# Kernel tuning notes

Hardware: AMD Instinct MI355X
Metric: run time of the kernel (lower is better)

Reference implementation:

```python
import jax, jax.numpy as jnp
import numpy as np

# Hyperparameters from __init__ defaults / chosen init kwargs
GAMMA_NEG = 4.0
GAMMA_POS = 1.0
CLIP = 0.05
EPS = 1e-8
ALPHA1 = 2.0
ALPHA_OTHER = 0.5
TOP_K = 10

B, C = 2048, 9605


def setup_inputs() -> dict:
    key = jax.random.key(0)
    k_x, k_y, k_c, k_r, k_d, k_o = jax.random.split(key, 6)
    x = jax.random.normal(k_x, (B, C), dtype=jnp.float32)
    y = (jax.random.uniform(k_y, (B, C)) < 0.01).astype(jnp.float32)
    compost_idx = jax.random.randint(k_c, (30,), 0, C, dtype=jnp.int32)
    recycle_idx = jax.random.randint(k_r, (70,), 0, C, dtype=jnp.int32)
    donate_idx = jax.random.randint(k_d, (70,), 0, C, dtype=jnp.int32)
    other_idx = jax.random.randint(k_o, (40,), 0, C, dtype=jnp.int32)
    # dense whitelist mapping: 0 = not in W_human mapping; priority compost>recycle>donate
    wl_map = jnp.zeros((C,), dtype=jnp.int32)
    wl_map = wl_map.at[other_idx].set(4)
    wl_map = wl_map.at[donate_idx].set(3)
    wl_map = wl_map.at[recycle_idx].set(2)
    wl_map = wl_map.at[compost_idx].set(1)
    return {"x": x, "y": y, "compost_idx": compost_idx,
            "recycle_idx": recycle_idx, "donate_idx": donate_idx,
            "wl_map": wl_map}


def reference(x, y, compost_idx, recycle_idx, donate_idx, wl_map):
    b, c = x.shape
    xs_pos = jax.nn.sigmoid(x)
    xs_neg = jnp.minimum(1.0 - xs_pos + CLIP, 1.0)  # clip shift, clamp max=1
    # base asymmetric BCE term: y*log(p) + (1-y)*log(1-p+clip)
    base = (y * jnp.log(jnp.maximum(xs_pos, EPS))
            + (1.0 - y) * jnp.log(jnp.maximum(xs_neg, EPS)))  # [B, C]

    # per-sample ground-truth whitelist groups (find_gt_whitelist)
    has1 = jnp.sum(y[:, compost_idx], axis=1) > 0  # [B]
    has2 = jnp.sum(y[:, recycle_idx], axis=1) > 0
    has3 = jnp.sum(y[:, donate_idx], axis=1) > 0
    gt_only4 = ~(has1 | has2 | has3)  # gt_whitelist == [4]

    # top-10 predicted classes (argsort descending, first 10)
    _, top_idx = jax.lax.top_k(xs_pos, TOP_K)  # [B, 10]
    rows = jnp.arange(b)

    def step(carry, j):
        # j: [B] class index at current rank; sequential over rank (order matters)
        mult, found = carry
        wl = wl_map[j]                      # group id of this class, 0 if unmapped
        in_map = wl > 0
        in_gt = (((wl == 1) & has1) | ((wl == 2) & has2)
                 | ((wl == 3) & has3) | ((wl == 4) & gt_only4))
        f = jnp.where(in_map & gt_only4, ALPHA_OTHER, 1.0)
        f = f * jnp.where(in_map & (~in_gt) & (~found), ALPHA1, 1.0)
        mult = mult.at[rows, j].multiply(f)
        found = found | (in_map & in_gt)
        return (mult, found), None

    init = (jnp.ones((b, c), x.dtype), jnp.zeros((b,), dtype=bool))
    (mult, found), _ = jax.lax.scan(step, init, top_idx.T)  # scan over 10 ranks

    # if no gt-whitelist match found in top-10: multiply all top-10 by alpha1 again
    extra = jnp.where(found[:, None], 1.0, ALPHA1)  # [B, 1]
    mult = mult.at[rows[:, None], top_idx].multiply(
        jnp.broadcast_to(extra, (b, TOP_K)))

    # asymmetric focal weighting (computed without grad in original)
    pt = xs_pos * y + xs_neg * (1.0 - y)
    gamma = GAMMA_POS * y + GAMMA_NEG * (1.0 - y)
    w = jax.lax.stop_gradient(jnp.power(1.0 - pt, gamma))

    return -jnp.sum(base * mult * w)
```

## Files before the change

### kernel.cpp

```cpp
#include <hip/hip_runtime.h>

#define TOPK 10
#define CLIP 0.05f
#define EPSV 1e-8f
#define ALPHA1 2.0f
#define ALPHA_OTHER 0.5f

__device__ __forceinline__ unsigned long long pack_vc(float v, int c, int C) {
  unsigned u = __float_as_uint(v);
  unsigned key = (u & 0x80000000u) ? ~u : (u | 0x80000000u);
  return ((unsigned long long)key << 32) | (unsigned)(C - c);
}
__device__ __forceinline__ float unpack_v(unsigned long long p) {
  unsigned key = (unsigned)(p >> 32);
  unsigned u = (key & 0x80000000u) ? (key & 0x7fffffffu) : ~key;
  return __uint_as_float(u);
}
__device__ __forceinline__ int unpack_c(unsigned long long p, int C) {
  return C - (int)(unsigned)(p & 0xffffffffu);
}

__device__ __forceinline__ float base_w(float xv, bool pos) {
  float p = 1.f / (1.f + __expf(-xv));
  float xneg = fminf(1.f - p + CLIP, 1.f);
  float q = pos ? p : xneg;
  float b = __logf(fmaxf(q, EPSV));
  float t = 1.f - q;
  float t2 = t * t;
  float w = pos ? t : t2 * t2;
  return b * w;
}

__global__ __launch_bounds__(256) void asl_kernel(
    const float* __restrict__ x, const float* __restrict__ y,
    const int* __restrict__ compost, const int* __restrict__ recycle,
    const int* __restrict__ donate, const int* __restrict__ wl_map,
    float* __restrict__ out, int C, int n1, int n2, int n3)
{
  const int row = blockIdx.x;
  const float* xr = x + (size_t)row * (size_t)C;
  const float* yr = y + (size_t)row * (size_t)C;
  const int tid = threadIdx.x;
  const int lane = tid & 63;
  const int wave = tid >> 6;

  __shared__ int s_has[3];
  __shared__ unsigned long long s_wl[4][TOPK];
  __shared__ float s_sum[4];

  if (tid < 3) s_has[tid] = 0;
  __syncthreads();

  const int ntot = n1 + n2 + n3;
  for (int i = tid; i < ntot; i += 256) {
    int which, colI;
    if (i < n1)            { which = 0; colI = compost[i]; }
    else if (i < n1 + n2)  { which = 1; colI = recycle[i - n1]; }
    else                   { which = 2; colI = donate[i - n1 - n2]; }
    if (yr[colI] > 0.5f) s_has[which] = 1;
  }

  float lv[TOPK]; int lc[TOPK];
#pragma unroll
  for (int s = 0; s < TOPK; s++) { lv[s] = -__builtin_inff(); lc[s] = 0; }

  float sum = 0.f;
  for (int col = tid; col < C; col += 256) {
    float xv = xr[col];
    float yv = yr[col];
    sum += base_w(xv, yv > 0.5f);
    if (xv > lv[TOPK - 1]) {
      float v = xv; int c = col;
#pragma unroll
      for (int s = 0; s < TOPK; s++) {
        bool g = v > lv[s];
        float tv = g ? lv[s] : v; int tc = g ? lc[s] : c;
        lv[s] = g ? v : lv[s];   lc[s] = g ? c : lc[s];
        v = tv; c = tc;
      }
    }
  }

#pragma unroll
  for (int off = 32; off > 0; off >>= 1) sum += __shfl_xor(sum, off, 64);
  if (lane == 0) s_sum[wave] = sum;

  for (int r = 0; r < TOPK; r++) {
    unsigned long long mine = pack_vc(lv[0], lc[0], C);
    unsigned long long best = mine;
#pragma unroll
    for (int off = 32; off > 0; off >>= 1) {
      unsigned long long o = __shfl_xor(best, off, 64);
      best = (o > best) ? o : best;
    }
    if (lane == 0) s_wl[wave][r] = best;
    if (mine == best) {
#pragma unroll
      for (int s = 0; s < TOPK - 1; s++) { lv[s] = lv[s + 1]; lc[s] = lc[s + 1]; }
      lv[TOPK - 1] = -__builtin_inff(); lc[TOPK - 1] = 0;
    }
  }
  __syncthreads();

  if (tid == 0) {
    float total = s_sum[0] + s_sum[1] + s_sum[2] + s_sum[3];
    const bool h1 = s_has[0] != 0, h2 = s_has[1] != 0, h3 = s_has[2] != 0;
    const bool gt4 = !(h1 || h2 || h3);

    unsigned long long top[TOPK];
    int p0 = 0, p1 = 0, p2 = 0, p3 = 0;
#pragma unroll
    for (int r = 0; r < TOPK; r++) {
      unsigned long long v0 = (p0 < TOPK) ? s_wl[0][p0] : 0ULL;
      unsigned long long v1 = (p1 < TOPK) ? s_wl[1][p1] : 0ULL;
      unsigned long long v2 = (p2 < TOPK) ? s_wl[2][p2] : 0ULL;
      unsigned long long v3 = (p3 < TOPK) ? s_wl[3][p3] : 0ULL;
      unsigned long long bv = v0; int bw_ = 0;
      if (v1 > bv) { bv = v1; bw_ = 1; }
      if (v2 > bv) { bv = v2; bw_ = 2; }
      if (v3 > bv) { bv = v3; bw_ = 3; }
      top[r] = bv;
      if (bw_ == 0) p0++; else if (bw_ == 1) p1++; else if (bw_ == 2) p2++; else p3++;
    }

    bool found = false;
    float fr[TOPK];
#pragma unroll
    for (int r = 0; r < TOPK; r++) {
      int col = unpack_c(top[r], C);
      int wl = wl_map[col];
      bool in_map = wl > 0;
      bool in_gt = (wl == 1 && h1) || (wl == 2 && h2) ||
                   (wl == 3 && h3) || (wl == 4 && gt4);
      float f = 1.f;
      if (in_map && gt4) f *= ALPHA_OTHER;
      if (in_map && !in_gt && !found) f *= ALPHA1;
      fr[r] = f;
      found = found || (in_map && in_gt);
    }
    const float extra = found ? 1.f : ALPHA1;
#pragma unroll
    for (int r = 0; r < TOPK; r++) {
      float mult = fr[r] * extra;
      if (mult != 1.f) {
        int col = unpack_c(top[r], C);
        float xv = unpack_v(top[r]);
        float bwv = base_w(xv, yr[col] > 0.5f);
        total += (mult - 1.f) * bwv;
      }
    }
    atomicAdd(out, -total);
  }
}

extern "C" void kernel_launch(void* const* d_in, const int* in_sizes, int n_in,
                              void* d_out, int out_size, void* d_ws, size_t ws_size,
                              hipStream_t stream) {
  const float* x       = (const float*)d_in[0];
  const float* y       = (const float*)d_in[1];
  const int*   compost = (const int*)d_in[2];
  const int*   recycle = (const int*)d_in[3];
  const int*   donate  = (const int*)d_in[4];
  const int*   wl_map  = (const int*)d_in[5];
  float* out = (float*)d_out;

  const int C  = in_sizes[5];
  const int B  = in_sizes[0] / C;
  const int n1 = in_sizes[2], n2 = in_sizes[3], n3 = in_sizes[4];

  hipMemsetAsync(out, 0, sizeof(float), stream);
  asl_kernel<<<B, 256, 0, stream>>>(x, y, compost, recycle, donate, wl_map,
                                    out, C, n1, n2, n3);
}
```

Measured before the change: 240.4 us.

## Replace per-thread top-k insertion with threshold candidate filtering and float4 loads

Instead of keeping a per-thread sorted top-10 list during the main pass, each thread appends values above a fixed threshold (2.5) to a shared candidate buffer via an LDS atomic. One wave then selects the top-10 from the candidates, falling back to a full rescan of the row when there are too few or too many. The main loop also moves to float4 vectorized loads with scalar head and tail handling. This removes divergent insertion work and register pressure from the streaming pass, at the cost of an extra barrier and an occasional serial fallback scan.

Measured after the change: 214.2 us. 10.9% less time.

```diff
diff --git a/kernel.cpp b/kernel.cpp
--- a/kernel.cpp
+++ b/kernel.cpp
@@ -5,6 +5,8 @@
 #define EPSV 1e-8f
 #define ALPHA1 2.0f
 #define ALPHA_OTHER 0.5f
+#define TCAND 2.5f
+#define MAXC 512
 
 __device__ __forceinline__ unsigned long long pack_vc(float v, int c, int C) {
   unsigned u = __float_as_uint(v);
@@ -45,10 +47,13 @@
   const int wave = tid >> 6;
 
   __shared__ int s_has[3];
-  __shared__ unsigned long long s_wl[4][TOPK];
+  __shared__ unsigned s_cnt;
+  __shared__ unsigned long long s_cand[MAXC];
   __shared__ float s_sum[4];
+  __shared__ unsigned long long s_top[TOPK];
 
   if (tid < 3) s_has[tid] = 0;
+  if (tid == 0) s_cnt = 0;
   __syncthreads();
 
   const int ntot = n1 + n2 + n3;
@@ -60,44 +65,83 @@
     if (yr[colI] > 0.5f) s_has[which] = 1;
   }
 
-  float lv[TOPK]; int lc[TOPK];
-#pragma unroll
-  for (int s = 0; s < TOPK; s++) { lv[s] = -__builtin_inff(); lc[s] = 0; }
-
   float sum = 0.f;
-  for (int col = tid; col < C; col += 256) {
-    float xv = xr[col];
-    float yv = yr[col];
-    sum += base_w(xv, yv > 0.5f);
-    if (xv > lv[TOPK - 1]) {
-      float v = xv; int c = col;
-#pragma unroll
-      for (int s = 0; s < TOPK; s++) {
-        bool g = v > lv[s];
-        float tv = g ? lv[s] : v; int tc = g ? lc[s] : c;
-        lv[s] = g ? v : lv[s];   lc[s] = g ? c : lc[s];
-        v = tv; c = tc;
-      }
-    }
-  }
+#define PROCESS(XV, YV, COL)                                              \
+  do {                                                                    \
+    float _xv = (XV);                                                     \
+    sum += base_w(_xv, (YV) > 0.5f);                                      \
+    if (_xv > TCAND) {                                                    \
+      unsigned _i = atomicAdd(&s_cnt, 1u);                                \
+      if (_i < MAXC) s_cand[_i] = pack_vc(_xv, (COL), C);                 \
+    }                                                                     \
+  } while (0)
+
+  int lead = (int)((4u - ((unsigned)((size_t)row * (size_t)C) & 3u)) & 3u);
+  if (lead > C) lead = C;
+  for (int col = tid; col < lead; col += 256) PROCESS(xr[col], yr[col], col);
+
+  const int nvec = (C - lead) >> 2;
+  const float4* __restrict__ x4 = (const float4*)(xr + lead);
+  const float4* __restrict__ y4 = (const float4*)(yr + lead);
+  for (int i = tid; i < nvec; i += 256) {
+    float4 xv = x4[i];
+    float4 yv = y4[i];
+    int cb = lead + i * 4;
+    PROCESS(xv.x, yv.x, cb + 0);
+    PROCESS(xv.y, yv.y, cb + 1);
+    PROCESS(xv.z, yv.z, cb + 2);
+    PROCESS(xv.w, yv.w, cb + 3);
+  }
+  for (int col = lead + nvec * 4 + tid; col < C; col += 256)
+    PROCESS(xr[col], yr[col], col);
+#undef PROCESS
 
 #pragma unroll
   for (int off = 32; off > 0; off >>= 1) sum += __shfl_xor(sum, off, 64);
   if (lane == 0) s_sum[wave] = sum;
-
-  for (int r = 0; r < TOPK; r++) {
-    unsigned long long mine = pack_vc(lv[0], lc[0], C);
-    unsigned long long best = mine;
-#pragma unroll
-    for (int off = 32; off > 0; off >>= 1) {
-      unsigned long long o = __shfl_xor(best, off, 64);
-      best = (o > best) ? o : best;
-    }
-    if (lane == 0) s_wl[wave][r] = best;
-    if (mine == best) {
-#pragma unroll
-      for (int s = 0; s < TOPK - 1; s++) { lv[s] = lv[s + 1]; lc[s] = lc[s + 1]; }
-      lv[TOPK - 1] = -__builtin_inff(); lc[TOPK - 1] = 0;
+  __syncthreads();
+
+  if (wave == 0) {
+    const unsigned cnt = s_cnt;
+    unsigned long long ls[TOPK];
+#pragma unroll
+    for (int s = 0; s < TOPK; s++) ls[s] = 0ULL;
+
+#define INSERT(P)                                                          \
+    do {                                                                   \
+      unsigned long long _p = (P);                                         \
+      if (_p > ls[TOPK - 1]) {                                             \
+        _Pragma("unroll")                                                  \
+        for (int _s = 0; _s < TOPK; _s++) {                                \
+          bool _g = _p > ls[_s];                                           \
+          unsigned long long _t = _g ? ls[_s] : _p;                        \
+          ls[_s] = _g ? _p : ls[_s];                                       \
+          _p = _t;                                                         \
+        }                                                                  \
+      }                                                                    \
+    } while (0)
+
+    if (cnt >= TOPK && cnt <= MAXC) {
+      for (unsigned i = lane; i < cnt; i += 64) INSERT(s_cand[i]);
+    } else {
+      for (int col = lane; col < C; col += 64) INSERT(pack_vc(xr[col], col, C));
+    }
+#undef INSERT
+
+    for (int r = 0; r < TOPK; r++) {
+      unsigned long long mine = ls[0];
+      unsigned long long best = mine;
+#pragma unroll
+      for (int off = 32; off > 0; off >>= 1) {
+        unsigned long long o = __shfl_xor(best, off, 64);
+        best = (o > best) ? o : best;
+      }
+      if (lane == 0) s_top[r] = best;
+      if (mine == best) {
+#pragma unroll
+        for (int s = 0; s < TOPK - 1; s++) ls[s] = ls[s + 1];
+        ls[TOPK - 1] = 0ULL;
+      }
     }
   }
   __syncthreads();
@@ -107,27 +151,11 @@
     const bool h1 = s_has[0] != 0, h2 = s_has[1] != 0, h3 = s_has[2] != 0;
     const bool gt4 = !(h1 || h2 || h3);
 
-    unsigned long long top[TOPK];
-    int p0 = 0, p1 = 0, p2 = 0, p3 = 0;
-#pragma unroll
-    for (int r = 0; r < TOPK; r++) {
-      unsigned long long v0 = (p0 < TOPK) ? s_wl[0][p0] : 0ULL;
-      unsigned long long v1 = (p1 < TOPK) ? s_wl[1][p1] : 0ULL;
-      unsigned long long v2 = (p2 < TOPK) ? s_wl[2][p2] : 0ULL;
-      unsigned long long v3 = (p3 < TOPK) ? s_wl[3][p3] : 0ULL;
-      unsigned long long bv = v0; int bw_ = 0;
-      if (v1 > bv) { bv = v1; bw_ = 1; }
-      if (v2 > bv) { bv = v2; bw_ = 2; }
-      if (v3 > bv) { bv = v3; bw_ = 3; }
-      top[r] = bv;
-      if (bw_ == 0) p0++; else if (bw_ == 1) p1++; else if (bw_ == 2) p2++; else p3++;
-    }
-
     bool found = false;
     float fr[TOPK];
 #pragma unroll
     for (int r = 0; r < TOPK; r++) {
-      int col = unpack_c(top[r], C);
+      int col = unpack_c(s_top[r], C);
       int wl = wl_map[col];
       bool in_map = wl > 0;
       bool in_gt = (wl == 1 && h1) || (wl == 2 && h2) ||
@@ -143,8 +171,8 @@
     for (int r = 0; r < TOPK; r++) {
       float mult = fr[r] * extra;
       if (mult != 1.f) {
-        int col = unpack_c(top[r], C);
-        float xv = unpack_v(top[r]);
+        int col = unpack_c(s_top[r], C);
+        float xv = unpack_v(s_top[r]);
         float bwv = base_w(xv, yr[col] > 0.5f);
         total += (mult - 1.f) * bwv;
       }
```
